# Optimization experiments

Hardware: AMD Instinct MI355X
Metric: run time of the kernel (lower is better)

The kernel has to match this reference:

```python
import jax, jax.numpy as jnp
import numpy as np

B = 2097152  # flattened batch of 3x3 rotation matrices

def setup_inputs() -> dict:
    key = jax.random.key(0)
    k1, k2 = jax.random.split(key)
    # scale by 0.1 so cos=(trace(m1 m2^T)-1)/2 stays strictly inside (-1,1)
    pred_rot = jax.random.normal(k1, (B, 3, 3), dtype=jnp.float32) * 0.1
    gt_rot = jax.random.normal(k2, (B, 3, 3), dtype=jnp.float32) * 0.1
    return {"pred_rot": pred_rot, "gt_rot": gt_rot}

def reference(pred_rot, gt_rot):
    m1 = pred_rot.reshape(-1, 3, 3)
    m2 = gt_rot.reshape(-1, 3, 3)
    # trace(m1 @ m2^T) == sum(m1 * m2) elementwise -> avoid the bmm
    cos = (jnp.einsum('bij,bij->b', m1, m2) - 1.0) * 0.5
    cos = jnp.clip(cos, -1.0, 1.0)  # min with +1, max with -1
    theta = jnp.arccos(cos)
    return jnp.mean(theta)  # reduction='mean'
```

## Files before the change

kernel.cpp:

```cpp
#include <hip/hip_runtime.h>
#include <math.h>


#define TPB 256
#define NBLOCKS 2048

__global__ __launch_bounds__(TPB) void geo_kernel(
    const float* __restrict__ a, const float* __restrict__ b,
    float* __restrict__ out, float invM, int M)
{
    __shared__ float wsum[TPB / 64];
    const int tid = threadIdx.x;
    const int q   = tid & 3;

    float sum = 0.0f;

    const long long G    = (long long)M >> 2;
    const long long Q0   = (long long)blockIdx.x * (TPB / 4) + (tid >> 2);
    const long long Qstr = (long long)gridDim.x * (TPB / 4);

    const float4* __restrict__ a4 = (const float4*)a;
    const float4* __restrict__ b4 = (const float4*)b;

    for (long long Q = Q0; Q < G; Q += Qstr) {
        const float4* __restrict__ pa = a4 + 9 * Q;
        const float4* __restrict__ pb = b4 + 9 * Q;
        const float4 A0 = pa[q], A1 = pa[4 + q], A2 = pa[8];
        const float4 B0 = pb[q], B1 = pb[4 + q], B2 = pb[8];

        float4 t0, t1;
        t0.x = A0.x * B0.x; t0.y = A0.y * B0.y;
        t0.z = A0.z * B0.z; t0.w = A0.w * B0.w;
        t1.x = A1.x * B1.x; t1.y = A1.y * B1.y;
        t1.z = A1.z * B1.z; t1.w = A1.w * B1.w;

        const float c01 = t0.x + t0.y;
        const float T0  = (c01 + t0.z) + t0.w;
        const float d01 = t1.x + t1.y;
        const float T1  = (d01 + t1.z) + t1.w;

        float P0 = (q == 3) ? 0.0f : ((q == 2) ? t0.x : T0);
        float P1 = (q == 0) ? d01  : ((q == 1) ? 0.0f
                   : ((q == 2) ? (T0 - t0.x) : T0));
        float P2 = (q == 0) ? (T1 - d01) : ((q == 1) ? T1
                   : ((q == 2) ? (T1 - t1.w) : 0.0f));
        float P3 = (q == 2) ? t1.w : ((q == 3) ? T1 : 0.0f);

        P0 += __shfl_xor(P0, 1, 64); P0 += __shfl_xor(P0, 2, 64);
        P1 += __shfl_xor(P1, 1, 64); P1 += __shfl_xor(P1, 2, 64);
        P2 += __shfl_xor(P2, 1, 64); P2 += __shfl_xor(P2, 2, 64);
        P3 += __shfl_xor(P3, 1, 64); P3 += __shfl_xor(P3, 2, 64);

        const float u0 = A2.x * B2.x, u1 = A2.y * B2.y;
        const float u2 = A2.z * B2.z, u3 = A2.w * B2.w;
        const float dl2 = (u0 + u1) + (u2 + u3);

        const float d = (q == 0) ? P0 : (q == 1) ? P1
                      : (q == 2) ? P2 : (P3 + dl2);
        const float cv = fminf(1.0f, fmaxf(-1.0f, (d - 1.0f) * 0.5f));
        sum += acosf(cv);
    }

    {
        const long long gid    = (long long)blockIdx.x * TPB + tid;
        const long long stride = (long long)gridDim.x * TPB;
        for (long long m = 4 * G + gid; m < M; m += stride) {
            float d = 0.0f;
            #pragma unroll
            for (int j = 0; j < 9; ++j)
                d = fmaf(a[m * 9 + j], b[m * 9 + j], d);
            sum += acosf(fminf(1.0f, fmaxf(-1.0f, (d - 1.0f) * 0.5f)));
        }
    }

    #pragma unroll
    for (int off = 32; off > 0; off >>= 1)
        sum += __shfl_down(sum, off, 64);
    if ((tid & 63) == 0) wsum[tid >> 6] = sum;
    __syncthreads();
    if (tid == 0) {
        float s = 0.0f;
        #pragma unroll
        for (int i = 0; i < TPB / 64; ++i) s += wsum[i];
        atomicAdd(out, s * invM);
    }
}

extern "C" void kernel_launch(void* const* d_in, const int* in_sizes, int n_in,
                              void* d_out, int out_size, void* d_ws, size_t ws_size,
                              hipStream_t stream) {
    const float* a = (const float*)d_in[0];
    const float* b = (const float*)d_in[1];
    float* out = (float*)d_out;

    const int n = in_sizes[0];
    const int M = n / 9;

    hipMemsetAsync(out, 0, (size_t)out_size * sizeof(float), stream);
    geo_kernel<<<NBLOCKS, TPB, 0, stream>>>(a, b, out, 1.0f / (float)M, M);
}
```

Before: 171.3 us.

## Software-prefetch next iteration with nontemporal loads and replace atomic with two-pass reduction

The main loop now issues the next iteration's loads, marked nontemporal, before computing the current one. This double-buffers registers to hide memory latency. The final reduction writes per-block partials to the workspace and runs a small finish kernel instead of a memset plus atomicAdd, falling back to the old path if the workspace is too small. This adds register pressure and one extra kernel launch in exchange for removing the memset and atomic contention.

Result: faster. 162.7 us (-5.0%).

```diff
diff --git a/kernel.cpp b/kernel.cpp
--- a/kernel.cpp
+++ b/kernel.cpp
@@ -2,12 +2,23 @@
 #include <math.h>
 
 
+typedef float f4 __attribute__((ext_vector_type(4)));
+
 #define TPB 256
 #define NBLOCKS 2048
 
-__global__ __launch_bounds__(TPB) void geo_kernel(
+#define LOADQ(P, pa, pb)                                                    \
+    P##A0 = __builtin_nontemporal_load((pa) + q);                           \
+    P##A1 = __builtin_nontemporal_load((pa) + 4 + q);                       \
+    P##A2 = __builtin_nontemporal_load((pa) + 8);                           \
+    P##B0 = __builtin_nontemporal_load((pb) + q);                           \
+    P##B1 = __builtin_nontemporal_load((pb) + 4 + q);                       \
+    P##B2 = __builtin_nontemporal_load((pb) + 8);
+
+__global__ __launch_bounds__(TPB) void geo_partial(
     const float* __restrict__ a, const float* __restrict__ b,
-    float* __restrict__ out, float invM, int M)
+    float* __restrict__ ws, float* __restrict__ out, float invM, int M,
+    int use_atomic)
 {
     __shared__ float wsum[TPB / 64];
     const int tid = threadIdx.x;
@@ -19,16 +30,27 @@
     const long long Q0   = (long long)blockIdx.x * (TPB / 4) + (tid >> 2);
     const long long Qstr = (long long)gridDim.x * (TPB / 4);
 
-    const float4* __restrict__ a4 = (const float4*)a;
-    const float4* __restrict__ b4 = (const float4*)b;
+    const f4* __restrict__ a4 = (const f4*)a;
+    const f4* __restrict__ b4 = (const f4*)b;
 
-    for (long long Q = Q0; Q < G; Q += Qstr) {
-        const float4* __restrict__ pa = a4 + 9 * Q;
-        const float4* __restrict__ pb = b4 + 9 * Q;
-        const float4 A0 = pa[q], A1 = pa[4 + q], A2 = pa[8];
-        const float4 B0 = pb[q], B1 = pb[4 + q], B2 = pb[8];
+    f4 A0, A1, A2, B0, B1, B2;
+    long long Q = Q0;
+    if (Q < G) {
+        const f4* pa = a4 + 9 * Q;
+        const f4* pb = b4 + 9 * Q;
+        LOADQ(, pa, pb)
+    }
 
-        float4 t0, t1;
+    while (Q < G) {
+        const long long Qn = Q + Qstr;
+        f4 NA0, NA1, NA2, NB0, NB1, NB2;
+        if (Qn < G) {
+            const f4* pa = a4 + 9 * Qn;
+            const f4* pb = b4 + 9 * Qn;
+            LOADQ(N, pa, pb)
+        }
+
+        f4 t0, t1;
         t0.x = A0.x * B0.x; t0.y = A0.y * B0.y;
         t0.z = A0.z * B0.z; t0.w = A0.w * B0.w;
         t1.x = A1.x * B1.x; t1.y = A1.y * B1.y;
@@ -59,17 +81,23 @@
                       : (q == 2) ? P2 : (P3 + dl2);
         const float cv = fminf(1.0f, fmaxf(-1.0f, (d - 1.0f) * 0.5f));
         sum += acosf(cv);
+
+        if (Qn < G) {
+            A0 = NA0; A1 = NA1; A2 = NA2;
+            B0 = NB0; B1 = NB1; B2 = NB2;
+        }
+        Q = Qn;
     }
 
     {
         const long long gid    = (long long)blockIdx.x * TPB + tid;
         const long long stride = (long long)gridDim.x * TPB;
         for (long long m = 4 * G + gid; m < M; m += stride) {
-            float d = 0.0f;
+            float dd = 0.0f;
             #pragma unroll
             for (int j = 0; j < 9; ++j)
-                d = fmaf(a[m * 9 + j], b[m * 9 + j], d);
-            sum += acosf(fminf(1.0f, fmaxf(-1.0f, (d - 1.0f) * 0.5f)));
+                dd = fmaf(a[m * 9 + j], b[m * 9 + j], dd);
+            sum += acosf(fminf(1.0f, fmaxf(-1.0f, (dd - 1.0f) * 0.5f)));
         }
     }
 
@@ -82,8 +110,25 @@
         float s = 0.0f;
         #pragma unroll
         for (int i = 0; i < TPB / 64; ++i) s += wsum[i];
-        atomicAdd(out, s * invM);
+        if (use_atomic) atomicAdd(out, s * invM);
+        else            ws[blockIdx.x] = s;
     }
+}
+
+__global__ __launch_bounds__(256) void geo_finish(
+    const float* __restrict__ ws, float* __restrict__ out,
+    float invM, int nb)
+{
+    __shared__ float wsum[4];
+    float s = 0.0f;
+    for (int i = threadIdx.x; i < nb; i += 256) s += ws[i];
+    #pragma unroll
+    for (int off = 32; off > 0; off >>= 1)
+        s += __shfl_down(s, off, 64);
+    if ((threadIdx.x & 63) == 0) wsum[threadIdx.x >> 6] = s;
+    __syncthreads();
+    if (threadIdx.x == 0)
+        out[0] = (wsum[0] + wsum[1] + wsum[2] + wsum[3]) * invM;
 }
 
 extern "C" void kernel_launch(void* const* d_in, const int* in_sizes, int n_in,
@@ -96,6 +141,14 @@
     const int n = in_sizes[0];
     const int M = n / 9;
 
-    hipMemsetAsync(out, 0, (size_t)out_size * sizeof(float), stream);
-    geo_kernel<<<NBLOCKS, TPB, 0, stream>>>(a, b, out, 1.0f / (float)M, M);
+    const bool ws_ok = (ws_size >= (size_t)NBLOCKS * sizeof(float));
+    if (!ws_ok) {
+        hipMemsetAsync(out, 0, (size_t)out_size * sizeof(float), stream);
+    }
+    geo_partial<<<NBLOCKS, TPB, 0, stream>>>(
+        a, b, (float*)d_ws, out, 1.0f / (float)M, M, ws_ok ? 0 : 1);
+    if (ws_ok) {
+        geo_finish<<<1, 256, 0, stream>>>(
+            (const float*)d_ws, out, 1.0f / (float)M, NBLOCKS);
+    }
 }
```
